# Kernel tuning notes

Hardware: AMD Instinct MI355X
Metric: run time of the kernel (lower is better)

The kernel has to match this reference:

```python
import jax, jax.numpy as jnp
import numpy as np

EPS_GN = 1e-5
DEN_MIN = 1e-4

B, C, H, W = 16, 256, 128, 128
MEM, NH = 64, 4
HD = MEM // NH
GROUPS = min(8, C // 4)


def setup_inputs() -> dict:
    key = jax.random.key(0)
    ks = jax.random.split(key, 12)
    s = 0.02
    x = jax.random.normal(ks[0], (B, C, H, W), jnp.float32)
    gn_w = jnp.ones((C,), jnp.float32)
    gn_b = jnp.zeros((C,), jnp.float32)
    Wk = jax.random.normal(ks[1], (MEM, C), jnp.float32) * s
    Wv = jax.random.normal(ks[2], (MEM, C), jnp.float32) * s
    Wq = jax.random.normal(ks[3], (MEM, C), jnp.float32) * s
    Wo = jax.random.normal(ks[4], (C, MEM), jnp.float32) * s
    bo = jnp.zeros((C,), jnp.float32)
    M0 = jax.random.normal(ks[5], (NH, HD, HD), jnp.float32) * s  # meta-learned warm start
    Z0 = jnp.ones((NH, HD), jnp.float32) * 0.1
    g1_w = jax.random.normal(ks[6], (C // 4, C), jnp.float32) * s
    g1_b = jnp.zeros((C // 4,), jnp.float32)
    g2_w = jax.random.normal(ks[7], (1, C // 4), jnp.float32) * s
    g2_b = jnp.full((1,), -2.0, jnp.float32)  # gate_bias
    return {"x": x, "gn_w": gn_w, "gn_b": gn_b, "Wk": Wk, "Wv": Wv, "Wq": Wq,
            "Wo": Wo, "bo": bo, "M0": M0, "Z0": Z0,
            "g1_w": g1_w, "g1_b": g1_b, "g2_w": g2_w, "g2_b": g2_b}


def _group_norm(x, w, b):
    b_, c, h, wd = x.shape
    xg = x.reshape(b_, GROUPS, c // GROUPS, h, wd)
    mu = jnp.mean(xg, axis=(2, 3, 4), keepdims=True)
    var = jnp.var(xg, axis=(2, 3, 4), keepdims=True)
    xn = ((xg - mu) * jax.lax.rsqrt(var + EPS_GN)).reshape(b_, c, h, wd)
    return xn * w[None, :, None, None] + b[None, :, None, None]


def _conv1x1(x, w):
    # x: (B,C,H,W), w: (O,C) -> (B,O,H,W)
    return jnp.einsum('bchw,oc->bohw', x, w)


def reference(x, gn_w, gn_b, Wk, Wv, Wq, Wo, bo, M0, Z0, g1_w, g1_b, g2_w, g2_b):
    bsz, c, h, w = x.shape
    n = h * w
    residual = x
    x_norm = _group_norm(x, gn_w, gn_b)

    k = _conv1x1(x_norm, Wk).reshape(bsz, NH, HD, n)
    v = _conv1x1(x_norm, Wv).reshape(bsz, NH, HD, n)
    q = _conv1x1(x_norm, Wq).reshape(bsz, NH, HD, n)

    phi_k = jax.nn.elu(k) + 1.0
    phi_q = jax.nn.elu(q) + 1.0

    M = jnp.einsum('bhdn,bhen->bhde', phi_k, v) + M0[None]
    Z = phi_k.sum(axis=-1) + Z0[None]
    y_num = jnp.einsum('bhde,bhdn->bhen', M, phi_q)
    y_den = jnp.einsum('bhd,bhdn->bhn', Z, phi_q)
    y_den = jnp.maximum(y_den, DEN_MIN)[:, :, None, :]
    y = (y_num / y_den).reshape(bsz, MEM, h, w)

    y = _conv1x1(y, Wo) + bo[None, :, None, None]

    # gate: global avg pool -> Linear -> GELU (exact) -> Linear -> sigmoid
    pooled = jnp.mean(x_norm, axis=(2, 3))  # (B, C)
    g = jax.nn.gelu(pooled @ g1_w.T + g1_b, approximate=False)
    gate = jax.nn.sigmoid(g @ g2_w.T + g2_b).reshape(bsz, 1, 1, 1)

    return residual + gate * y, gate
```

## Files before the change

### kernel.cpp

```cpp
#include <hip/hip_runtime.h>
#include <math.h>

typedef __attribute__((ext_vector_type(8))) short short8b;
typedef __attribute__((ext_vector_type(4))) float f32x4;

#define B_   16
#define C_   256
#define N_   16384
#define NH_  4
#define G_   8
#define CPG_ 32

#define OFF_S    0
#define OFF_T    4096
#define OFF_SUM  OFF_S
#define OFF_SQ   OFF_T
#define OFF_M    8192
#define OFF_Z    24576
#define OFF_GATE 25600
#define OFF_WKVQ 25616

static __device__ inline unsigned short bf16u(float f) {
    unsigned int u = __float_as_uint(f);
    return (unsigned short)((u + 0x7FFFu + ((u >> 16) & 1u)) >> 16);
}
static __device__ inline float ubf(unsigned short u) {
    return __uint_as_float(((unsigned int)u) << 16);
}

__global__ __launch_bounds__(256) void k_stats(const float* __restrict__ x,
                                               float* __restrict__ ws) {
    const int bc = blockIdx.x;
    const float4* p4 = (const float4*)(x + (size_t)bc * N_);
    float s = 0.f, q = 0.f;
    #pragma unroll 4
    for (int i = threadIdx.x; i < N_ / 4; i += 256) {
        float4 v = p4[i];
        s += v.x + v.y + v.z + v.w;
        q += v.x * v.x + v.y * v.y + v.z * v.z + v.w * v.w;
    }
    #pragma unroll
    for (int o = 32; o > 0; o >>= 1) {
        s += __shfl_down(s, o);
        q += __shfl_down(q, o);
    }
    __shared__ float ls[4], lq[4];
    const int wid = threadIdx.x >> 6, lane = threadIdx.x & 63;
    if (lane == 0) { ls[wid] = s; lq[wid] = q; }
    __syncthreads();
    if (threadIdx.x == 0) {
        ws[OFF_SUM + bc] = ls[0] + ls[1] + ls[2] + ls[3];
        ws[OFF_SQ  + bc] = lq[0] + lq[1] + lq[2] + lq[3];
    }
}

__global__ __launch_bounds__(256) void k_cvtw(const float* __restrict__ Wk,
        const float* __restrict__ Wv, const float* __restrict__ Wq,
        float* __restrict__ ws) {
    unsigned short* wkvq = (unsigned short*)(ws + OFF_WKVQ);
    const int r = blockIdx.x, t = threadIdx.x;
    const float* src = r < 64 ? Wk + r * C_
                     : r < 128 ? Wv + (r - 64) * C_
                     : Wq + (r - 128) * C_;
    wkvq[r * 256 + t] = bf16u(src[t]);
}

__global__ __launch_bounds__(256) void k_prep(
        const float* __restrict__ gnw, const float* __restrict__ gnb,
        const float* __restrict__ M0,  const float* __restrict__ Z0,
        const float* __restrict__ g1w, const float* __restrict__ g1b,
        const float* __restrict__ g2w, const float* __restrict__ g2b,
        float* __restrict__ ws, float* __restrict__ out_gate) {
    const int b = blockIdx.x, t = threadIdx.x;
    __shared__ float mu[G_], rs[G_];
    __shared__ float pooled[C_];
    __shared__ float hidden[64];

    if (t < G_) {
        float S = 0.f, Q = 0.f;
        for (int c = t * CPG_; c < (t + 1) * CPG_; ++c) {
            S += ws[OFF_SUM + b * C_ + c];
            Q += ws[OFF_SQ  + b * C_ + c];
        }
        const float cnt = (float)(CPG_ * N_);
        const float m = S / cnt;
        const float var = Q / cnt - m * m;
        mu[t] = m;
        rs[t] = rsqrtf(var + 1e-5f);
    }
    __syncthreads();
    {
        const int c = t;
        const int g = c / CPG_;
        const float sumc = ws[OFF_SUM + b * C_ + c];
        const float sc = rs[g] * gnw[c];
        const float tc = gnb[c] - mu[g] * sc;
        ws[OFF_S + b * C_ + c] = sc;
        ws[OFF_T + b * C_ + c] = tc;
        pooled[c] = fmaf(sumc * (1.f / (float)N_), sc, tc);
    }
    __syncthreads();
    if (t < 64) {
        float a = g1b[t];
        for (int c = 0; c < C_; ++c) a = fmaf(pooled[c], g1w[t * C_ + c], a);
        hidden[t] = 0.5f * a * (1.f + erff(a * 0.70710678118654752f));
    }
    __syncthreads();
    if (t == 0) {
        float z = g2b[0];
        for (int j = 0; j < 64; ++j) z = fmaf(hidden[j], g2w[j], z);
        const float gate = 1.f / (1.f + expf(-z));
        ws[OFF_GATE + b] = gate;
        out_gate[b] = gate;
    }
    for (int i = t; i < NH_ * 256; i += 256) ws[OFF_M + b * 1024 + i] = M0[i];
    for (int i = t; i < 64;        i += 256) ws[OFF_Z + b * 64 + i]   = Z0[i];
}

__global__ __launch_bounds__(256) void k_projmz(const float* __restrict__ x,
                                                float* __restrict__ ws) {
    __shared__ __align__(16) char lds[35072];
    char* w_s = lds;
    char* x_s = lds + 10240;
    unsigned short (*kvt)[136] = (unsigned short (*)[136])lds;
    float* z_red = (float*)(lds + 34816);

    const int b = blockIdx.y, px0 = blockIdx.x * 128;
    const int t = threadIdx.x, w = t >> 6, l = t & 63;
    const float* __restrict__ sv = ws + OFF_S + b * C_;
    const float* __restrict__ tv = ws + OFF_T + b * C_;
    const unsigned int* __restrict__ wkvq32 = (const unsigned int*)(ws + OFF_WKVQ);
    const float* __restrict__ xb = x + (size_t)b * C_ * N_ + px0;

    if (t < 64) z_red[t] = 0.f;

    f32x4 acc[2][8];
    #pragma unroll
    for (int i = 0; i < 2; ++i)
        #pragma unroll
        for (int j = 0; j < 8; ++j) acc[i][j] = (f32x4){0.f, 0.f, 0.f, 0.f};

    for (int ks = 0; ks < 8; ++ks) {
        __syncthreads();
        #pragma unroll
        for (int i = 0; i < 8; ++i) {
            const int e2 = t + 256 * i;
            const int row = e2 >> 4, kp = e2 & 15;
            *(unsigned int*)(w_s + row * 80 + kp * 4) =
                wkvq32[row * 128 + ks * 16 + kp];
        }
        {
            const int px = t & 127, half = t >> 7;
            #pragma unroll
            for (int i = 0; i < 8; ++i) {
                const int lc = half * 16 + i * 2;
                const int c = ks * 32 + lc;
                const float a0 = fmaf(xb[(size_t)c * N_ + px],       sv[c],     tv[c]);
                const float a1 = fmaf(xb[(size_t)(c + 1) * N_ + px], sv[c + 1], tv[c + 1]);
                *(unsigned int*)(x_s + px * 80 + lc * 2) =
                    ((unsigned int)bf16u(a1) << 16) | bf16u(a0);
            }
        }
        __syncthreads();
        short8b bfr[8];
        #pragma unroll
        for (int ct = 0; ct < 8; ++ct)
            bfr[ct] = *(const short8b*)(x_s + (ct * 16 + (l & 15)) * 80 + (l >> 4) * 16);
        #pragma unroll
        for (int rt = 0; rt < 2; ++rt) {
            const int row = w * 32 + rt * 16 + (l & 15);
            const short8b af = *(const short8b*)(w_s + row * 80 + (l >> 4) * 16);
            #pragma unroll
            for (int ct = 0; ct < 8; ++ct)
                acc[rt][ct] = __builtin_amdgcn_mfma_f32_16x16x32_bf16(
                                  af, bfr[ct], acc[rt][ct], 0, 0, 0);
        }
    }
    __syncthreads();

    #pragma unroll
    for (int rt = 0; rt < 2; ++rt) {
        const int base = w * 32 + rt * 16;
        const bool do_elu = base < 64;
        #pragma unroll
        for (int ct = 0; ct < 8; ++ct) {
            const int px = ct * 16 + (l & 15);
            #pragma unroll
            for (int r = 0; r < 4; ++r) {
                const int row = base + (l >> 4) * 4 + r;
                float v = acc[rt][ct][r];
                if (do_elu) v = v > 0.f ? v + 1.f : __expf(v);
                kvt[row][px] = bf16u(v);
            }
        }
    }
    __syncthreads();

    f32x4 accm = (f32x4){0.f, 0.f, 0.f, 0.f};
    #pragma unroll
    for (int kc = 0; kc < 4; ++kc) {
        const short8b af = *(const short8b*)((const char*)&kvt[w * 16 + (l & 15)][0]
                                             + kc * 64 + (l >> 4) * 16);
        const short8b bf = *(const short8b*)((const char*)&kvt[64 + w * 16 + (l & 15)][0]
                                             + kc * 64 + (l >> 4) * 16);
        accm = __builtin_amdgcn_mfma_f32_16x16x32_bf16(af, bf, accm, 0, 0, 0);
    }
    {
        const int zrow = t >> 2, zq = t & 3;
        float z = 0.f;
        #pragma unroll
        for (int j = 0; j < 16; ++j) {
            const unsigned int u = *(const unsigned int*)&kvt[zrow][zq * 32 + j * 2];
            z += ubf((unsigned short)u) + ubf((unsigned short)(u >> 16));
        }
        atomicAdd(&z_red[zrow], z);
    }
    #pragma unroll
    for (int r = 0; r < 4; ++r) {
        const int d = (l >> 4) * 4 + r, e = l & 15;
        atomicAdd(&ws[OFF_M + b * 1024 + w * 256 + d * 16 + e], accm[r]);
    }
    __syncthreads();
    if (t < 64) atomicAdd(&ws[OFF_Z + b * 64 + t], z_red[t]);
}

__global__ __launch_bounds__(512, 4) void k_out5(const float* __restrict__ x,
        const float* __restrict__ Wo, const float* __restrict__ bo,
        const float* __restrict__ ws, float* __restrict__ out) {
    __shared__ __align__(16) char lds[74752];
    char*  pq_s = lds;
    char*  breg = lds + 32768;
    float* bo_s = (float*)(lds + 73728);

    const int b = blockIdx.y, px0 = blockIdx.x * 256;
    const int t = threadIdx.x, w = t >> 6, l = t & 63;
    const int h = w >> 1;
    const int pxw = (w & 1) * 128;
    const float* __restrict__ sv = ws + OFF_S + b * C_;
    const float* __restrict__ tv = ws + OFF_T + b * C_;
    const unsigned short* __restrict__ wkvq16 = (const unsigned short*)(ws + OFF_WKVQ);
    const float* __restrict__ xb = x + (size_t)b * C_ * N_ + px0;

    if (t < 256) bo_s[t] = bo[t];
    float* m_s = (float*)pq_s;
    for (int i = t; i < 1024; i += 512) m_s[i] = ws[OFF_M + b * 1024 + i];
    float zr[4];
    #pragma unroll
    for (int r = 0; r < 4; ++r)
        zr[r] = ws[OFF_Z + b * 64 + h * 16 + (l >> 4) * 4 + r];

    short8b afq[8];
    {
        const unsigned short* wq = wkvq16
            + (size_t)(128 + h * 16 + (l & 15)) * 256 + (l >> 4) * 8;
        #pragma unroll
        for (int ks = 0; ks < 8; ++ks) afq[ks] = *(const short8b*)(wq + ks * 32);
    }

    const int px_ = t & 255, half = t >> 8;
    char* xs0 = breg;
    char* xs1 = breg + 20480;

    f32x4 accq[8];
    #pragma unroll
    for (int j = 0; j < 8; ++j) accq[j] = (f32x4){0.f, 0.f, 0.f, 0.f};

    {
        float xf[16];
        #pragma unroll
        for (int i = 0; i < 16; ++i)
            xf[i] = xb[(size_t)(half * 16 + i) * N_ + px_];
        #pragma unroll
        for (int i = 0; i < 8; ++i) {
            const int c = half * 16 + 2 * i;
            const float a0 = fmaf(xf[2 * i],     sv[c],     tv[c]);
            const float a1 = fmaf(xf[2 * i + 1], sv[c + 1], tv[c + 1]);
            *(unsigned int*)(xs0 + px_ * 80 + (half * 16 + 2 * i) * 2) =
                ((unsigned int)bf16u(a1) << 16) | bf16u(a0);
        }
    }
    __syncthreads();
    #pragma unroll
    for (int ks = 0; ks < 8; ++ks) {
        char* xcur = (ks & 1) ? xs1 : xs0;
        char* xnxt = (ks & 1) ? xs0 : xs1;
        float xg[16];
        if (ks < 7) {
            #pragma unroll
            for (int i = 0; i < 16; ++i)
                xg[i] = xb[(size_t)((ks + 1) * 32 + half * 16 + i) * N_ + px_];
        }
        #pragma unroll
        for (int ct = 0; ct < 8; ++ct) {
            const short8b bfr = *(const short8b*)(xcur + (pxw + ct * 16 + (l & 15)) * 80
                                                  + (l >> 4) * 16);
            accq[ct] = __builtin_amdgcn_mfma_f32_16x16x32_bf16(
                           afq[ks], bfr, accq[ct], 0, 0, 0);
        }
        if (ks < 7) {
            #pragma unroll
            for (int i = 0; i < 8; ++i) {
                const int c = (ks + 1) * 32 + half * 16 + 2 * i;
                const float a0 = fmaf(xg[2 * i],     sv[c],     tv[c]);
                const float a1 = fmaf(xg[2 * i + 1], sv[c + 1], tv[c + 1]);
                *(unsigned int*)(xnxt + px_ * 80 + (half * 16 + 2 * i) * 2) =
                    ((unsigned int)bf16u(a1) << 16) | bf16u(a0);
            }
        }
        __syncthreads();
    }

    char* w2_s = breg;
    {
        const int c = t & 255, hp = t >> 8;
        #pragma unroll
        for (int hh = 0; hh < 2; ++hh) {
            const int hw = hp * 2 + hh;
            float wrow[16];
            #pragma unroll
            for (int j = 0; j < 4; ++j)
                *(float4*)&wrow[j * 4] = *(const float4*)&Wo[c * 64 + hw * 16 + j * 4];
            float av[16];
            #pragma unroll
            for (int d = 0; d < 16; ++d) {
                float a = 0.f;
                #pragma unroll
                for (int e = 0; e < 16; ++e)
                    a = fmaf(wrow[e], m_s[hw * 256 + d * 16 + e], a);
                av[d] = a;
            }
            #pragma unroll
            for (int j = 0; j < 8; ++j) {
                const unsigned int pk = (unsigned int)bf16u(av[2 * j])
                                      | ((unsigned int)bf16u(av[2 * j + 1]) << 16);
                *(unsigned int*)(w2_s + c * 128 + ((hw * 32 + j * 4) ^ ((c & 7) << 4))) = pk;
            }
        }
    }
    __syncthreads();

    #pragma unroll
    for (int ct = 0; ct < 8; ++ct) {
        float p[4];
        #pragma unroll
        for (int r = 0; r < 4; ++r) {
            const float v = accq[ct][r];
            p[r] = v > 0.f ? v + 1.f : __expf(v);
        }
        float dp = 0.f;
        #pragma unroll
        for (int r = 0; r < 4; ++r) dp = fmaf(zr[r], p[r], dp);
        dp += __shfl_xor(dp, 16);
        dp += __shfl_xor(dp, 32);
        const float rd = 1.f / fmaxf(dp, 1e-4f);
        const int px = pxw + ct * 16 + (l & 15);
        const unsigned int lo = (unsigned int)bf16u(p[0] * rd)
                              | ((unsigned int)bf16u(p[1] * rd) << 16);
        const unsigned int hi = (unsigned int)bf16u(p[2] * rd)
                              | ((unsigned int)bf16u(p[3] * rd) << 16);
        const int off = (h * 32 + (l >> 4) * 8) ^ ((px & 7) << 4);
        *(unsigned long long*)(pq_s + px * 128 + off) =
            (unsigned long long)lo | ((unsigned long long)hi << 32);
    }
    __syncthreads();

    const float gate = ws[OFF_GATE + b];
    const float* __restrict__ xr = x + (size_t)b * C_ * N_ + px0;
    float* __restrict__ ob = out + (size_t)b * C_ * N_ + px0;
    #pragma unroll
    for (int rt = 0; rt < 4; ++rt) {
        f32x4 acc[8];
        #pragma unroll
        for (int j = 0; j < 8; ++j) acc[j] = (f32x4){0.f, 0.f, 0.f, 0.f};
        const int row = h * 64 + rt * 16 + (l & 15);
        #pragma unroll
        for (int ksi = 0; ksi < 2; ++ksi) {
            const short8b af = *(const short8b*)(w2_s + row * 128
                                 + ((ksi * 64 + (l >> 4) * 16) ^ ((row & 7) << 4)));
            #pragma unroll
            for (int ct = 0; ct < 8; ++ct) {
                const int px = pxw + ct * 16 + (l & 15);
                const short8b bfr = *(const short8b*)(pq_s + px * 128
                                 + ((ksi * 64 + (l >> 4) * 16) ^ ((px & 7) << 4)));
                acc[ct] = __builtin_amdgcn_mfma_f32_16x16x32_bf16(
                              af, bfr, acc[ct], 0, 0, 0);
            }
        }
        #pragma unroll
        for (int ct = 0; ct < 8; ++ct) {
            const int px = pxw + ct * 16 + (l & 15);
            #pragma unroll
            for (int r = 0; r < 4; ++r) {
                const int orow = h * 64 + rt * 16 + (l >> 4) * 4 + r;
                const size_t off = (size_t)orow * N_ + px;
                ob[off] = fmaf(gate, acc[ct][r] + bo_s[orow], xr[off]);
            }
        }
    }
}

extern "C" void kernel_launch(void* const* d_in, const int* in_sizes, int n_in,
                              void* d_out, int out_size, void* d_ws, size_t ws_size,
                              hipStream_t stream) {
    const float* x   = (const float*)d_in[0];
    const float* gnw = (const float*)d_in[1];
    const float* gnb = (const float*)d_in[2];
    const float* Wk  = (const float*)d_in[3];
    const float* Wv  = (const float*)d_in[4];
    const float* Wq  = (const float*)d_in[5];
    const float* Wo  = (const float*)d_in[6];
    const float* bo  = (const float*)d_in[7];
    const float* M0  = (const float*)d_in[8];
    const float* Z0  = (const float*)d_in[9];
    const float* g1w = (const float*)d_in[10];
    const float* g1b = (const float*)d_in[11];
    const float* g2w = (const float*)d_in[12];
    const float* g2b = (const float*)d_in[13];
    float* out = (float*)d_out;
    float* ws  = (float*)d_ws;

    hipLaunchKernelGGL(k_stats,  dim3(B_ * C_), dim3(256), 0, stream, x, ws);
    hipLaunchKernelGGL(k_cvtw,   dim3(192),     dim3(256), 0, stream, Wk, Wv, Wq, ws);
    hipLaunchKernelGGL(k_prep,   dim3(B_),      dim3(256), 0, stream,
                       gnw, gnb, M0, Z0, g1w, g1b, g2w, g2b, ws,
                       out + (size_t)B_ * C_ * N_);
    hipLaunchKernelGGL(k_projmz, dim3(N_ / 128, B_), dim3(256), 0, stream, x, ws);
    hipLaunchKernelGGL(k_out5,   dim3(N_ / 256, B_), dim3(512), 0, stream,
                       x, Wo, bo, ws, out);
}
```

Measured before the change: 302.0 us.

## Halve pixel tile in output kernel and shrink LDS for higher occupancy

The output kernel now handles 128 pixels per block instead of 256, which halves the per-wave accumulator arrays. LDS is cut from about 73KB to about 49KB by reusing one region for the x staging buffers, the M matrix and the normalized phi_q tile. The x staging layout drops its 80-byte padded rows for 64-byte rows with an XOR swizzle. Launch bounds go from 4 to 6 blocks per CU, aiming to hide latency with more resident waves. The cost is twice as many blocks, each recomputing the Wo·M product and reloading M and weights, plus an extra barrier.

```diff
diff --git a/kernel.cpp b/kernel.cpp
--- a/kernel.cpp
+++ b/kernel.cpp
@@ -224,26 +224,24 @@
     if (t < 64) atomicAdd(&ws[OFF_Z + b * 64 + t], z_red[t]);
 }
 
-__global__ __launch_bounds__(512, 4) void k_out5(const float* __restrict__ x,
+__global__ __launch_bounds__(512, 6) void k_out6(const float* __restrict__ x,
         const float* __restrict__ Wo, const float* __restrict__ bo,
         const float* __restrict__ ws, float* __restrict__ out) {
-    __shared__ __align__(16) char lds[74752];
-    char*  pq_s = lds;
-    char*  breg = lds + 32768;
-    float* bo_s = (float*)(lds + 73728);
-
-    const int b = blockIdx.y, px0 = blockIdx.x * 256;
+    __shared__ __align__(16) char lds[50176];
+    char*  regA = lds;
+    char*  w2_s = lds + 16384;
+    float* bo_s = (float*)(lds + 49152);
+
+    const int b = blockIdx.y, px0 = blockIdx.x * 128;
     const int t = threadIdx.x, w = t >> 6, l = t & 63;
     const int h = w >> 1;
-    const int pxw = (w & 1) * 128;
+    const int pxw = (w & 1) * 64;
     const float* __restrict__ sv = ws + OFF_S + b * C_;
     const float* __restrict__ tv = ws + OFF_T + b * C_;
     const unsigned short* __restrict__ wkvq16 = (const unsigned short*)(ws + OFF_WKVQ);
     const float* __restrict__ xb = x + (size_t)b * C_ * N_ + px0;
 
     if (t < 256) bo_s[t] = bo[t];
-    float* m_s = (float*)pq_s;
-    for (int i = t; i < 1024; i += 512) m_s[i] = ws[OFF_M + b * 1024 + i];
     float zr[4];
     #pragma unroll
     for (int r = 0; r < 4; ++r)
@@ -257,25 +255,26 @@
         for (int ks = 0; ks < 8; ++ks) afq[ks] = *(const short8b*)(wq + ks * 32);
     }
 
-    const int px_ = t & 255, half = t >> 8;
-    char* xs0 = breg;
-    char* xs1 = breg + 20480;
-
-    f32x4 accq[8];
-    #pragma unroll
-    for (int j = 0; j < 8; ++j) accq[j] = (f32x4){0.f, 0.f, 0.f, 0.f};
+    const int px_ = t & 127, q = t >> 7;
+    char* xs0 = regA;
+    char* xs1 = regA + 8192;
+    const int swzA = ((px_ >> 1) & 3) << 4;
+
+    f32x4 accq[4];
+    #pragma unroll
+    for (int j = 0; j < 4; ++j) accq[j] = (f32x4){0.f, 0.f, 0.f, 0.f};
 
     {
-        float xf[16];
-        #pragma unroll
-        for (int i = 0; i < 16; ++i)
-            xf[i] = xb[(size_t)(half * 16 + i) * N_ + px_];
-        #pragma unroll
-        for (int i = 0; i < 8; ++i) {
-            const int c = half * 16 + 2 * i;
-            const float a0 = fmaf(xf[2 * i],     sv[c],     tv[c]);
-            const float a1 = fmaf(xf[2 * i + 1], sv[c + 1], tv[c + 1]);
-            *(unsigned int*)(xs0 + px_ * 80 + (half * 16 + 2 * i) * 2) =
+        float xf[8];
+        #pragma unroll
+        for (int i = 0; i < 8; ++i)
+            xf[i] = xb[(size_t)(q * 8 + i) * N_ + px_];
+        #pragma unroll
+        for (int j = 0; j < 4; ++j) {
+            const int c = q * 8 + 2 * j;
+            const float a0 = fmaf(xf[2 * j],     sv[c],     tv[c]);
+            const float a1 = fmaf(xf[2 * j + 1], sv[c + 1], tv[c + 1]);
+            *(unsigned int*)(xs0 + px_ * 64 + ((q * 16 + 4 * j) ^ swzA)) =
                 ((unsigned int)bf16u(a1) << 16) | bf16u(a0);
         }
     }
@@ -284,33 +283,37 @@
     for (int ks = 0; ks < 8; ++ks) {
         char* xcur = (ks & 1) ? xs1 : xs0;
         char* xnxt = (ks & 1) ? xs0 : xs1;
-        float xg[16];
+        float xg[8];
         if (ks < 7) {
             #pragma unroll
-            for (int i = 0; i < 16; ++i)
-                xg[i] = xb[(size_t)((ks + 1) * 32 + half * 16 + i) * N_ + px_];
-        }
-        #pragma unroll
-        for (int ct = 0; ct < 8; ++ct) {
-            const short8b bfr = *(const short8b*)(xcur + (pxw + ct * 16 + (l & 15)) * 80
-                                                  + (l >> 4) * 16);
+            for (int i = 0; i < 8; ++i)
+                xg[i] = xb[(size_t)((ks + 1) * 32 + q * 8 + i) * N_ + px_];
+        }
+        #pragma unroll
+        for (int ct = 0; ct < 4; ++ct) {
+            const int px = pxw + ct * 16 + (l & 15);
+            const short8b bfr = *(const short8b*)(xcur + px * 64
+                                  + (((l >> 4) * 16) ^ (((px >> 1) & 3) << 4)));
             accq[ct] = __builtin_amdgcn_mfma_f32_16x16x32_bf16(
                            afq[ks], bfr, accq[ct], 0, 0, 0);
         }
         if (ks < 7) {
             #pragma unroll
-            for (int i = 0; i < 8; ++i) {
-                const int c = (ks + 1) * 32 + half * 16 + 2 * i;
-                const float a0 = fmaf(xg[2 * i],     sv[c],     tv[c]);
-                const float a1 = fmaf(xg[2 * i + 1], sv[c + 1], tv[c + 1]);
-                *(unsigned int*)(xnxt + px_ * 80 + (half * 16 + 2 * i) * 2) =
+            for (int j = 0; j < 4; ++j) {
+                const int c = (ks + 1) * 32 + q * 8 + 2 * j;
+                const float a0 = fmaf(xg[2 * j],     sv[c],     tv[c]);
+                const float a1 = fmaf(xg[2 * j + 1], sv[c + 1], tv[c + 1]);
+                *(unsigned int*)(xnxt + px_ * 64 + ((q * 16 + 4 * j) ^ swzA)) =
                     ((unsigned int)bf16u(a1) << 16) | bf16u(a0);
             }
         }
         __syncthreads();
     }
 
-    char* w2_s = breg;
+    float* m_s = (float*)regA;
+    for (int i = t; i < 1024; i += 512) m_s[i] = ws[OFF_M + b * 1024 + i];
+    __syncthreads();
+
     {
         const int c = t & 255, hp = t >> 8;
         #pragma unroll
@@ -339,8 +342,9 @@
     }
     __syncthreads();
 
-    #pragma unroll
-    for (int ct = 0; ct < 8; ++ct) {
+    char* pq_s = regA;
+    #pragma unroll
+    for (int ct = 0; ct < 4; ++ct) {
         float p[4];
         #pragma unroll
         for (int r = 0; r < 4; ++r) {
@@ -369,16 +373,16 @@
     float* __restrict__ ob = out + (size_t)b * C_ * N_ + px0;
     #pragma unroll
     for (int rt = 0; rt < 4; ++rt) {
-        f32x4 acc[8];
-        #pragma unroll
-        for (int j = 0; j < 8; ++j) acc[j] = (f32x4){0.f, 0.f, 0.f, 0.f};
+        f32x4 acc[4];
+        #pragma unroll
+        for (int j = 0; j < 4; ++j) acc[j] = (f32x4){0.f, 0.f, 0.f, 0.f};
         const int row = h * 64 + rt * 16 + (l & 15);
         #pragma unroll
         for (int ksi = 0; ksi < 2; ++ksi) {
             const short8b af = *(const short8b*)(w2_s + row * 128
                                  + ((ksi * 64 + (l >> 4) * 16) ^ ((row & 7) << 4)));
             #pragma unroll
-            for (int ct = 0; ct < 8; ++ct) {
+            for (int ct = 0; ct < 4; ++ct) {
                 const int px = pxw + ct * 16 + (l & 15);
                 const short8b bfr = *(const short8b*)(pq_s + px * 128
                                  + ((ksi * 64 + (l >> 4) * 16) ^ ((px & 7) << 4)));
@@ -387,7 +391,7 @@
             }
         }
         #pragma unroll
-        for (int ct = 0; ct < 8; ++ct) {
+        for (int ct = 0; ct < 4; ++ct) {
             const int px = pxw + ct * 16 + (l & 15);
             #pragma unroll
             for (int r = 0; r < 4; ++r) {
@@ -425,6 +429,6 @@
                        gnw, gnb, M0, Z0, g1w, g1b, g2w, g2b, ws,
                        out + (size_t)B_ * C_ * N_);
     hipLaunchKernelGGL(k_projmz, dim3(N_ / 128, B_), dim3(256), 0, stream, x, ws);
-    hipLaunchKernelGGL(k_out5,   dim3(N_ / 256, B_), dim3(512), 0, stream,
+    hipLaunchKernelGGL(k_out6,   dim3(N_ / 128, B_), dim3(512), 0, stream,
                        x, Wo, bo, ws, out);
 }
```

Result: slower. 348.2 us (+15.3%).
